# Kernel optimization log

Hardware: AMD Instinct MI355X
Metric: run time of the kernel (lower is better)

Reference implementation:

```python
import jax, jax.numpy as jnp
import numpy as np

N, F, E = 10000, 128, 640000
HID_RO = 64


def setup_inputs() -> dict:
    key = jax.random.key(0)
    ks = jax.random.split(key, 16)
    s = 1.0 / np.sqrt(F)
    inp = {
        'h': jax.random.normal(ks[0], (N, F), jnp.float32),
        'src_idx': jax.random.randint(ks[1], (E,), 0, N, jnp.int32),
        'dst_idx': jax.random.randint(ks[2], (E,), 0, N, jnp.int32),
        # message-creation MLP (F -> F -> F)
        'W1': jax.random.normal(ks[3], (F, F), jnp.float32) * s,
        'b1': jnp.zeros((F,), jnp.float32),
        'W2': jax.random.normal(ks[4], (F, F), jnp.float32) * s,
        'b2': jnp.zeros((F,), jnp.float32),
        # attention aggregation kernels
        'node_kernel': jax.random.normal(ks[5], (F, F), jnp.float32) * s,
        'attn_kernel': jax.random.normal(ks[6], (2 * F, 1), jnp.float32) * s,
        # feed-forward update (agg + h -> new h)
        'Wu': jax.random.normal(ks[7], (2 * F, F), jnp.float32) * s,
        'bu': jnp.zeros((F,), jnp.float32),
        # readout MLP (F -> 64 -> 1)
        'Wr1': jax.random.normal(ks[8], (F, HID_RO), jnp.float32) * s,
        'br1': jnp.zeros((HID_RO,), jnp.float32),
        'Wr2': jax.random.normal(ks[9], (HID_RO, 1), jnp.float32) * (1.0 / np.sqrt(HID_RO)),
        'br2': jnp.zeros((1,), jnp.float32),
    }
    return inp


def reference(h, src_idx, dst_idx, W1, b1, W2, b2, node_kernel, attn_kernel,
              Wu, bu, Wr1, br1, Wr2, br2):
    n = h.shape[0]
    # per-edge gather + message-creation NN  [E, F]
    h_src = h[src_idx]
    m = jax.nn.relu(h_src @ W1 + b1) @ W2 + b2
    # attention aggregation (GAT-style): transform messages, score vs dst state
    wh = m @ node_kernel                      # [E, F]
    h_dst = h[dst_idx]                        # [E, F]
    e = jax.nn.leaky_relu(jnp.concatenate([wh, h_dst], axis=-1) @ attn_kernel,
                          negative_slope=0.2)[:, 0]  # [E]
    # per-destination segment softmax (numerically stable)
    e_max = jax.ops.segment_max(e, dst_idx, num_segments=n)
    ex = jnp.exp(e - e_max[dst_idx])
    denom = jax.ops.segment_sum(ex, dst_idx, num_segments=n)
    alpha = ex / (denom[dst_idx] + 1e-9)
    # scatter-reduce weighted messages into destination states  [N, F]
    agg = jax.ops.segment_sum(m * alpha[:, None], dst_idx, num_segments=n)
    # feed-forward update
    h_new = jax.nn.relu(jnp.concatenate([agg, h], axis=-1) @ Wu + bu)
    # readout MLP -> per-node scalar
    out = jax.nn.relu(h_new @ Wr1 + br1) @ Wr2 + br2  # [N, 1]
    return out
```

## Files before the change

### kernel.cpp

```cpp
#include <hip/hip_runtime.h>
#include <hip/hip_bf16.h>
#include <hip/hip_fp16.h>

#define F 128
#define HID 64
#define KMAX 4
#define DEG_CAP 256
#define NTM 16
#define NTU 16
#define CHUNK_LOG 13
#define CHUNK (1 << CHUNK_LOG)


__global__ __launch_bounds__(256) void fused_front(
    const int* __restrict__ dst, unsigned short* __restrict__ cnt,
    unsigned short* __restrict__ rank,
    int e, int n, int histBlocks,
    const float* __restrict__ h,
    const float* __restrict__ W1, const float* __restrict__ b1,
    const float* __restrict__ W2, const float* __restrict__ b2,
    const float* __restrict__ nk, const float* __restrict__ attn,
    __half* __restrict__ Mh, float* __restrict__ p, float* __restrict__ q)
{
    __shared__ __align__(16) int lhist[10240];
    int tid = threadIdx.x;

    if ((int)blockIdx.x < histBlocks) {
        int n4 = n >> 2;
        int4* lh4 = (int4*)lhist;
        for (int i = tid; i < n4; i += 256) lh4[i] = make_int4(0, 0, 0, 0);
        for (int i = (n4 << 2) + tid; i < n; i += 256) lhist[i] = 0;
        __syncthreads();

        int base = (int)blockIdx.x << CHUNK_LOG;
        int lim = min(e - base, CHUNK);
        int lim4 = lim >> 2;
        const int4* d4 = (const int4*)(dst + base);
        for (int k = tid; k < lim4; k += 256) {
            int4 dv = d4[k];
            ushort4 rv;
            rv.x = (unsigned short)atomicAdd(&lhist[dv.x], 1);
            rv.y = (unsigned short)atomicAdd(&lhist[dv.y], 1);
            rv.z = (unsigned short)atomicAdd(&lhist[dv.z], 1);
            rv.w = (unsigned short)atomicAdd(&lhist[dv.w], 1);
            *(ushort4*)&rank[base + 4 * k] = rv;
        }
        for (int k = (lim4 << 2) + tid; k < lim; k += 256)
            rank[base + k] = (unsigned short)atomicAdd(&lhist[dst[base + k]], 1);
        __syncthreads();

        unsigned int* crow = (unsigned int*)(cnt + (size_t)blockIdx.x * n);
        int nh = n >> 1;
        for (int i = tid; i < nh; i += 256) {
            unsigned int v = ((unsigned int)lhist[2 * i] & 0xffffu) |
                             ((unsigned int)lhist[2 * i + 1] << 16);
            crow[i] = v;
        }
        return;
    }

    float (*hsTs)[F] = (float (*)[F])lhist;
    float (*Wc)[F]   = (float (*)[F])((char*)lhist + 8192);
    float* v1s       = (float*)((char*)lhist + 24576);

    int bm = blockIdx.x - histBlocks;
    int row0 = bm * NTM;
    int j0 = (tid & 31) * 4;
    int r0 = (tid >> 5) * 2;

    #pragma unroll
    for (int it = 0; it < 2; ++it) {
        int s4 = tid + it * 256;
        int r = s4 >> 5, c4 = s4 & 31;
        int row = row0 + r;
        float4 v = make_float4(0, 0, 0, 0);
        if (row < n) v = *(const float4*)&h[(size_t)row * F + c4 * 4];
        *(float4*)&hsTs[r][c4 * 4] = v;
    }
    if (tid < F) {
        float a = 0.f;
        const float4* nkr = (const float4*)&nk[(size_t)tid * F];
        const float4* at4 = (const float4*)attn;
        #pragma unroll 8
        for (int j = 0; j < 32; ++j) {
            float4 nv = nkr[j]; float4 av = at4[j];
            a = fmaf(nv.x, av.x, a); a = fmaf(nv.y, av.y, a);
            a = fmaf(nv.z, av.z, a); a = fmaf(nv.w, av.w, a);
        }
        v1s[tid] = a;
    }
    __syncthreads();

    {
        int r = tid >> 4, kp = tid & 15;
        float qa = 0.f;
        #pragma unroll
        for (int c = 0; c < 2; ++c) {
            float4 hv = *(const float4*)&hsTs[r][kp * 8 + c * 4];
            float4 av = *(const float4*)&attn[F + kp * 8 + c * 4];
            qa = fmaf(hv.x, av.x, qa); qa = fmaf(hv.y, av.y, qa);
            qa = fmaf(hv.z, av.z, qa); qa = fmaf(hv.w, av.w, qa);
        }
        #pragma unroll
        for (int off = 1; off < 16; off <<= 1) qa += __shfl_xor(qa, off, 64);
        int row = row0 + r;
        if (kp == 0 && row < n) q[row] = qa;
    }

    float4 acc[2];
    {
        float4 bv = *(const float4*)&b1[j0];
        acc[0] = bv; acc[1] = bv;
    }
    for (int cc = 0; cc < 4; ++cc) {
        int kc = ((cc + bm) & 3) * 32;
        __syncthreads();
        #pragma unroll
        for (int it = 0; it < 4; ++it) {
            int s4 = tid + it * 256;
            int wr = s4 >> 5, wc4 = s4 & 31;
            *(float4*)&Wc[wr][wc4 * 4] =
                *(const float4*)&W1[(size_t)(kc + wr) * F + wc4 * 4];
        }
        __syncthreads();
        #pragma unroll
        for (int k4 = 0; k4 < 8; ++k4) {
            int kk = k4 * 4;
            float4 a0 = *(const float4*)&hsTs[r0 + 0][kc + kk];
            float4 a1 = *(const float4*)&hsTs[r0 + 1][kc + kk];
            #pragma unroll
            for (int k = 0; k < 4; ++k) {
                float4 b = *(const float4*)&Wc[kk + k][j0];
                float av0 = k == 0 ? a0.x : k == 1 ? a0.y : k == 2 ? a0.z : a0.w;
                float av1 = k == 0 ? a1.x : k == 1 ? a1.y : k == 2 ? a1.z : a1.w;
                acc[0].x = fmaf(av0, b.x, acc[0].x); acc[0].y = fmaf(av0, b.y, acc[0].y);
                acc[0].z = fmaf(av0, b.z, acc[0].z); acc[0].w = fmaf(av0, b.w, acc[0].w);
                acc[1].x = fmaf(av1, b.x, acc[1].x); acc[1].y = fmaf(av1, b.y, acc[1].y);
                acc[1].z = fmaf(av1, b.z, acc[1].z); acc[1].w = fmaf(av1, b.w, acc[1].w);
            }
        }
    }
    __syncthreads();
    #pragma unroll
    for (int i = 0; i < 2; ++i) {
        float4 t = acc[i];
        t.x = fmaxf(t.x, 0.f); t.y = fmaxf(t.y, 0.f);
        t.z = fmaxf(t.z, 0.f); t.w = fmaxf(t.w, 0.f);
        *(float4*)&hsTs[r0 + i][j0] = t;
    }

    {
        float4 bv = *(const float4*)&b2[j0];
        acc[0] = bv; acc[1] = bv;
    }
    for (int cc = 0; cc < 4; ++cc) {
        int kc = ((cc + bm) & 3) * 32;
        __syncthreads();
        #pragma unroll
        for (int it = 0; it < 4; ++it) {
            int s4 = tid + it * 256;
            int wr = s4 >> 5, wc4 = s4 & 31;
            *(float4*)&Wc[wr][wc4 * 4] =
                *(const float4*)&W2[(size_t)(kc + wr) * F + wc4 * 4];
        }
        __syncthreads();
        #pragma unroll
        for (int k4 = 0; k4 < 8; ++k4) {
            int kk = k4 * 4;
            float4 a0 = *(const float4*)&hsTs[r0 + 0][kc + kk];
            float4 a1 = *(const float4*)&hsTs[r0 + 1][kc + kk];
            #pragma unroll
            for (int k = 0; k < 4; ++k) {
                float4 b = *(const float4*)&Wc[kk + k][j0];
                float av0 = k == 0 ? a0.x : k == 1 ? a0.y : k == 2 ? a0.z : a0.w;
                float av1 = k == 0 ? a1.x : k == 1 ? a1.y : k == 2 ? a1.z : a1.w;
                acc[0].x = fmaf(av0, b.x, acc[0].x); acc[0].y = fmaf(av0, b.y, acc[0].y);
                acc[0].z = fmaf(av0, b.z, acc[0].z); acc[0].w = fmaf(av0, b.w, acc[0].w);
                acc[1].x = fmaf(av1, b.x, acc[1].x); acc[1].y = fmaf(av1, b.y, acc[1].y);
                acc[1].z = fmaf(av1, b.z, acc[1].z); acc[1].w = fmaf(av1, b.w, acc[1].w);
            }
        }
    }

    float4 v1v = *(const float4*)&v1s[j0];
    #pragma unroll
    for (int i = 0; i < 2; ++i) {
        int row = row0 + r0 + i;
        if (row < n) {
            __half hv[4];
            hv[0] = __float2half(acc[i].x); hv[1] = __float2half(acc[i].y);
            hv[2] = __float2half(acc[i].z); hv[3] = __float2half(acc[i].w);
            *(uint2*)&Mh[(size_t)row * F + j0] = *(uint2*)hv;
        }
        float pp = acc[i].x * v1v.x + acc[i].y * v1v.y +
                   acc[i].z * v1v.z + acc[i].w * v1v.w;
        #pragma unroll
        for (int off = 1; off < 32; off <<= 1) pp += __shfl_xor(pp, off, 64);
        if ((tid & 31) == 0 && row < n) p[row] = pp;
    }
}

__global__ __launch_bounds__(256) void scan_block(
    unsigned short* __restrict__ cnt, int* __restrict__ rstart,
    int* __restrict__ bsum, int n, int hb)
{
    int tid = threadIdx.x;
    int i = blockIdx.x * 256 + tid;
    int run = 0;
    if (i < n) {
        size_t stride = (size_t)n;
        size_t idx = (size_t)i;
        int r = 0;
        for (; r + 8 <= hb; r += 8) {
            int c0 = cnt[idx];
            int c1 = cnt[idx + stride];
            int c2 = cnt[idx + 2 * stride];
            int c3 = cnt[idx + 3 * stride];
            int c4 = cnt[idx + 4 * stride];
            int c5 = cnt[idx + 5 * stride];
            int c6 = cnt[idx + 6 * stride];
            int c7 = cnt[idx + 7 * stride];
            cnt[idx]              = (unsigned short)run;
            cnt[idx + stride]     = (unsigned short)(run + c0);
            cnt[idx + 2 * stride] = (unsigned short)(run + (c0 + c1));
            cnt[idx + 3 * stride] = (unsigned short)(run + (c0 + c1 + c2));
            cnt[idx + 4 * stride] = (unsigned short)(run + (c0 + c1 + c2 + c3));
            cnt[idx + 5 * stride] = (unsigned short)(run + (c0 + c1 + c2 + c3 + c4));
            cnt[idx + 6 * stride] = (unsigned short)(run + (c0 + c1 + c2 + c3 + c4 + c5));
            cnt[idx + 7 * stride] = (unsigned short)(run + (c0 + c1 + c2 + c3 + c4 + c5 + c6));
            run += c0 + c1 + c2 + c3 + c4 + c5 + c6 + c7;
            idx += 8 * stride;
        }
        for (; r < hb; ++r) {
            int c = cnt[idx];
            cnt[idx] = (unsigned short)run;
            run += c;
            idx += stride;
        }
    }
    int v = run;
    int lane = tid & 63, wv = tid >> 6;
    int x = v;
    #pragma unroll
    for (int off = 1; off < 64; off <<= 1) {
        int t = __shfl_up(x, off, 64);
        if (lane >= off) x += t;
    }
    __shared__ int wsum[4];
    if (lane == 63) wsum[wv] = x;
    __syncthreads();
    int woff = 0;
    #pragma unroll
    for (int wdx = 0; wdx < 4; ++wdx) woff += (wdx < wv) ? wsum[wdx] : 0;
    int incl = x + woff;
    if (i < n) rstart[i] = incl - v;
    if (tid == 255) bsum[blockIdx.x] = incl;
}

__global__ __launch_bounds__(256) void fill_kernel(
    const int* __restrict__ dst, const int* __restrict__ src,
    const unsigned short* __restrict__ rank, const int* __restrict__ rstart,
    const unsigned short* __restrict__ cntoff, const int* __restrict__ bsum,
    unsigned short* __restrict__ src_sorted, int n, int nb, int e)
{
    __shared__ int sbo[64];
    int tid = threadIdx.x;
    if (tid < 64) {
        int v = (tid < nb) ? bsum[tid] : 0;
        int x = v;
        #pragma unroll
        for (int off = 1; off < 64; off <<= 1) {
            int t = __shfl_up(x, off, 64);
            if (tid >= off) x += t;
        }
        sbo[tid] = x - v;
    }
    __syncthreads();
    int i = blockIdx.x * 256 + tid;
    if (i < e) {
        int d = dst[i];
        int rep = i >> CHUNK_LOG;
        int pos = rstart[d] + sbo[d >> 8] + (int)cntoff[(size_t)rep * n + d] + (int)rank[i];
        src_sorted[pos] = (unsigned short)src[i];
    }
}

__global__ __launch_bounds__(256) void agg_update(
    const __half* __restrict__ Mh, const float* __restrict__ p,
    const float* __restrict__ q, const int* __restrict__ rstart,
    const int* __restrict__ bsum, const unsigned short* __restrict__ src_sorted,
    const float* __restrict__ h,
    const float* __restrict__ Wu, const float* __restrict__ bu,
    const float* __restrict__ Wr1, const float* __restrict__ br1,
    const float* __restrict__ Wr2, const float* __restrict__ br2,
    float* __restrict__ out, int n, int nb, int e)
{
    __shared__ __align__(16) float smem[8192];
    float (*X)[2 * F] = (float (*)[2 * F])smem;
    int2* bufa = (int2*)&smem[4096];
    int*  sbo  = (int*)&smem[6144];

    int tid = threadIdx.x;
    int wv   = tid >> 6;
    int lane = tid & 63;
    int row0 = blockIdx.x * NTU;

    if (tid < 64) {
        int v = (tid < nb) ? bsum[tid] : 0;
        int x = v;
        #pragma unroll
        for (int off = 1; off < 64; off <<= 1) {
            int t = __shfl_up(x, off, 64);
            if (tid >= off) x += t;
        }
        sbo[tid] = x - v;
    }
    #pragma unroll
    for (int it = 0; it < 2; ++it) {
        int s4 = tid + it * 256;
        int r = s4 >> 5, c4 = s4 & 31;
        int row = row0 + r;
        float4 v = make_float4(0, 0, 0, 0);
        if (row < n) v = *(const float4*)&h[(size_t)row * F + c4 * 4];
        *(float4*)&X[r][128 + c4 * 4] = v;
    }
    __syncthreads();

    const uint4* M16 = (const uint4*)Mh;
    int sub16 = lane & 15;
    int quar  = lane >> 4;
    int2* bufw = bufa + wv * DEG_CAP;

    for (int s = 0; s < 4; ++s) {
        int lr = wv * 4 + s;
        int node = row0 + lr;
        if (node >= n) break;

        int start = rstart[node] + sbo[node >> 8];
        int end   = (node + 1 < n) ? rstart[node + 1] + sbo[(node + 1) >> 8] : e;
        int deg   = end - start;
        float qn  = q[node];

        float w[KMAX];
        int   sidx[KMAX];
        float lmax = -1e30f;

        #pragma unroll
        for (int k = 0; k < KMAX; ++k) {
            int i = start + lane + (k << 6);
            bool valid = (i < end);
            int sv = valid ? (int)src_sorted[i] : 0;
            float pv = valid ? p[sv] : 0.0f;
            float sc = pv + qn;
            float ev = (sc > 0.0f) ? sc : 0.2f * sc;
            w[k] = valid ? ev : -1e30f;
            sidx[k] = sv;
            lmax = fmaxf(lmax, w[k]);
        }
        for (int i = start + DEG_CAP + lane; i < end; i += 64) {
            float sc = p[(int)src_sorted[i]] + qn;
            float ev = (sc > 0.0f) ? sc : 0.2f * sc;
            lmax = fmaxf(lmax, ev);
        }
        #pragma unroll
        for (int off = 32; off >= 1; off >>= 1)
            lmax = fmaxf(lmax, __shfl_xor(lmax, off, 64));

        float lsum = 0.0f;
        #pragma unroll
        for (int k = 0; k < KMAX; ++k) {
            float ex = (w[k] > -1e29f) ? __expf(w[k] - lmax) : 0.0f;
            w[k] = ex;
            lsum += ex;
        }
        for (int i = start + DEG_CAP + lane; i < end; i += 64) {
            float sc = p[(int)src_sorted[i]] + qn;
            float ev = (sc > 0.0f) ? sc : 0.2f * sc;
            lsum += __expf(ev - lmax);
        }
        #pragma unroll
        for (int off = 32; off >= 1; off >>= 1)
            lsum += __shfl_xor(lsum, off, 64);
        float inv = 1.0f / (lsum + 1e-9f);

        #pragma unroll
        for (int k = 0; k < KMAX; ++k)
            bufw[lane + (k << 6)] = make_int2(__float_as_int(w[k] * inv), sidx[k]);

        float acc[8] = {0.f, 0.f, 0.f, 0.f, 0.f, 0.f, 0.f, 0.f};
        int lim = min(deg, DEG_CAP);
        lim = (lim + 15) & ~15;

        for (int base = 0; base < lim; base += 16) {
            int2  rr[4];
            uint4 mm[4];
            #pragma unroll
            for (int u = 0; u < 4; ++u) rr[u] = bufw[base + quar + 4 * u];
            #pragma unroll
            for (int u = 0; u < 4; ++u) mm[u] = M16[(size_t)rr[u].y * 16 + sub16];
            #pragma unroll
            for (int u = 0; u < 4; ++u) {
                float wu = __int_as_float(rr[u].x);
                const __half2* hp = (const __half2*)&mm[u];
                float2 f0 = __half22float2(hp[0]);
                float2 f1 = __half22float2(hp[1]);
                float2 f2 = __half22float2(hp[2]);
                float2 f3 = __half22float2(hp[3]);
                acc[0] = fmaf(wu, f0.x, acc[0]); acc[1] = fmaf(wu, f0.y, acc[1]);
                acc[2] = fmaf(wu, f1.x, acc[2]); acc[3] = fmaf(wu, f1.y, acc[3]);
                acc[4] = fmaf(wu, f2.x, acc[4]); acc[5] = fmaf(wu, f2.y, acc[5]);
                acc[6] = fmaf(wu, f3.x, acc[6]); acc[7] = fmaf(wu, f3.y, acc[7]);
            }
        }

        for (int base = start + DEG_CAP; base < end; base += 64) {
            int i = base + lane;
            float ex = 0.f; int sv = 0;
            if (i < end) {
                sv = (int)src_sorted[i];
                float sc = p[sv] + qn;
                float ev = (sc > 0.0f) ? sc : 0.2f * sc;
                ex = __expf(ev - lmax) * inv;
            }
            bufw[lane] = make_int2(__float_as_int(ex), sv);
            for (int b2 = 0; b2 < 64; b2 += 4) {
                int2 rr = bufw[b2 + quar];
                uint4 mm = M16[(size_t)rr.y * 16 + sub16];
                float wu = __int_as_float(rr.x);
                const __half2* hp = (const __half2*)&mm;
                float2 f0 = __half22float2(hp[0]);
                float2 f1 = __half22float2(hp[1]);
                float2 f2 = __half22float2(hp[2]);
                float2 f3 = __half22float2(hp[3]);
                acc[0] = fmaf(wu, f0.x, acc[0]); acc[1] = fmaf(wu, f0.y, acc[1]);
                acc[2] = fmaf(wu, f1.x, acc[2]); acc[3] = fmaf(wu, f1.y, acc[3]);
                acc[4] = fmaf(wu, f2.x, acc[4]); acc[5] = fmaf(wu, f2.y, acc[5]);
                acc[6] = fmaf(wu, f3.x, acc[6]); acc[7] = fmaf(wu, f3.y, acc[7]);
            }
        }

        #pragma unroll
        for (int j = 0; j < 8; ++j) {
            acc[j] += __shfl_xor(acc[j], 16, 64);
            acc[j] += __shfl_xor(acc[j], 32, 64);
        }
        if (quar == 0) {
            *(float4*)&X[lr][sub16 * 8]     = make_float4(acc[0], acc[1], acc[2], acc[3]);
            *(float4*)&X[lr][sub16 * 8 + 4] = make_float4(acc[4], acc[5], acc[6], acc[7]);
        }
    }
    __syncthreads();

    int j0 = (lane & 31) * 4;
    int rh = (lane >> 5) * 8;
    float4 acc[8];
    #pragma unroll
    for (int i = 0; i < 8; ++i) acc[i] = make_float4(0.f, 0.f, 0.f, 0.f);
    int kbase = wv * 64;
    for (int k4 = 0; k4 < 16; ++k4) {
        int kk = kbase + k4 * 4;
        float4 a[8];
        #pragma unroll
        for (int r = 0; r < 8; ++r) a[r] = *(const float4*)&X[rh + r][kk];
        #pragma unroll
        for (int k = 0; k < 4; ++k) {
            float4 b = *(const float4*)&Wu[(size_t)(kk + k) * F + j0];
            #pragma unroll
            for (int r = 0; r < 8; ++r) {
                float av = k == 0 ? a[r].x : k == 1 ? a[r].y : k == 2 ? a[r].z : a[r].w;
                acc[r].x = fmaf(av, b.x, acc[r].x);
                acc[r].y = fmaf(av, b.y, acc[r].y);
                acc[r].z = fmaf(av, b.z, acc[r].z);
                acc[r].w = fmaf(av, b.w, acc[r].w);
            }
        }
    }
    __syncthreads();

    #pragma unroll
    for (int r = 0; r < 8; ++r)
        *(float4*)&smem[wv * 2048 + (rh + r) * 128 + j0] = acc[r];
    __syncthreads();

    #pragma unroll
    for (int u = 0; u < 2; ++u) {
        int idx = tid * 2 + u;
        int row = idx >> 5, c4 = (idx & 31) * 4;
        float4 s0 = *(const float4*)&smem[0 * 2048 + row * 128 + c4];
        float4 s1 = *(const float4*)&smem[1 * 2048 + row * 128 + c4];
        float4 s2 = *(const float4*)&smem[2 * 2048 + row * 128 + c4];
        float4 s3 = *(const float4*)&smem[3 * 2048 + row * 128 + c4];
        float4 bv = *(const float4*)&bu[c4];
        float4 t;
        t.x = fmaxf(s0.x + s1.x + s2.x + s3.x + bv.x, 0.f);
        t.y = fmaxf(s0.y + s1.y + s2.y + s3.y + bv.y, 0.f);
        t.z = fmaxf(s0.z + s1.z + s2.z + s3.z + bv.z, 0.f);
        t.w = fmaxf(s0.w + s1.w + s2.w + s3.w + bv.w, 0.f);
        *(float4*)&smem[row * 128 + c4] = t;
    }
    __syncthreads();

    int h0 = (lane & 31) * 2;
    float r1a[8], r1b[8];
    #pragma unroll
    for (int r = 0; r < 8; ++r) { r1a[r] = 0.f; r1b[r] = 0.f; }
    int kb2 = wv * 32;
    for (int k4 = 0; k4 < 8; ++k4) {
        int kk = kb2 + k4 * 4;
        float4 a[8];
        #pragma unroll
        for (int r = 0; r < 8; ++r) a[r] = *(const float4*)&smem[(rh + r) * 128 + kk];
        #pragma unroll
        for (int k = 0; k < 4; ++k) {
            float2 b = *(const float2*)&Wr1[(size_t)(kk + k) * HID + h0];
            #pragma unroll
            for (int r = 0; r < 8; ++r) {
                float av = k == 0 ? a[r].x : k == 1 ? a[r].y : k == 2 ? a[r].z : a[r].w;
                r1a[r] = fmaf(av, b.x, r1a[r]);
                r1b[r] = fmaf(av, b.y, r1b[r]);
            }
        }
    }
    #pragma unroll
    for (int r = 0; r < 8; ++r) {
        smem[2048 + wv * 1024 + (rh + r) * 64 + h0]     = r1a[r];
        smem[2048 + wv * 1024 + (rh + r) * 64 + h0 + 1] = r1b[r];
    }
    __syncthreads();

    {
        int row = tid >> 4;
        int hp  = (tid & 15) * 4;
        float val = 0.f;
        #pragma unroll
        for (int j = 0; j < 4; ++j) {
            int hh = hp + j;
            float s = br1[hh]
                    + smem[2048 + 0 * 1024 + row * 64 + hh]
                    + smem[2048 + 1 * 1024 + row * 64 + hh]
                    + smem[2048 + 2 * 1024 + row * 64 + hh]
                    + smem[2048 + 3 * 1024 + row * 64 + hh];
            val = fmaf(fmaxf(s, 0.f), Wr2[hh], val);
        }
        #pragma unroll
        for (int off = 1; off < 16; off <<= 1) val += __shfl_xor(val, off, 64);
        int orow = row0 + row;
        if ((tid & 15) == 0 && orow < n) out[orow] = val + br2[0];
    }
}

extern "C" void kernel_launch(void* const* d_in, const int* in_sizes, int n_in,
                              void* d_out, int out_size, void* d_ws, size_t ws_size,
                              hipStream_t stream) {
    const float* h    = (const float*)d_in[0];
    const int*   src  = (const int*)d_in[1];
    const int*   dst  = (const int*)d_in[2];
    const float* W1   = (const float*)d_in[3];
    const float* b1   = (const float*)d_in[4];
    const float* W2   = (const float*)d_in[5];
    const float* b2   = (const float*)d_in[6];
    const float* nk   = (const float*)d_in[7];
    const float* attn = (const float*)d_in[8];
    const float* Wu   = (const float*)d_in[9];
    const float* bu   = (const float*)d_in[10];
    const float* Wr1  = (const float*)d_in[11];
    const float* br1  = (const float*)d_in[12];
    const float* Wr2  = (const float*)d_in[13];
    const float* br2  = (const float*)d_in[14];
    float* out = (float*)d_out;

    int n = in_sizes[0] / F;
    int e = in_sizes[1];
    int nb = (n + 255) / 256;
    int hb = (e + CHUNK - 1) >> CHUNK_LOG;
    int mlpBlocks  = (n + NTM - 1) / NTM;
    int fusBlocks  = (n + NTU - 1) / NTU;
    int fillBlocks = (e + 255) / 256;

    char* ws = (char*)d_ws;
    size_t off = 0;
    auto alloc = [&](size_t bytes) {
        void* pp = ws + off;
        off += (bytes + 511) & ~(size_t)511;
        return pp;
    };
    __half* Mh             = (__half*)alloc((size_t)n * F * 2);
    float* p               = (float*)alloc((size_t)n * 4);
    float* q               = (float*)alloc((size_t)n * 4);
    unsigned short* cnt    = (unsigned short*)alloc((size_t)hb * n * 2);
    int*   rstart          = (int*)alloc((size_t)(n + 1) * 4);
    int*   bsum            = (int*)alloc((size_t)(nb + 1) * 4);
    unsigned short* rank   = (unsigned short*)alloc((size_t)e * 2);
    unsigned short* srcsort= (unsigned short*)alloc((size_t)e * 2);

    fused_front<<<hb + mlpBlocks, 256, 0, stream>>>(
        dst, cnt, rank, e, n, hb,
        h, W1, b1, W2, b2, nk, attn, Mh, p, q);
    scan_block<<<nb, 256, 0, stream>>>(cnt, rstart, bsum, n, hb);
    fill_kernel<<<fillBlocks, 256, 0, stream>>>(dst, src, rank, rstart,
                                                cnt, bsum, srcsort,
                                                n, nb, e);
    agg_update<<<fusBlocks, 256, 0, stream>>>(Mh, p, q, rstart, bsum, srcsort,
                                              h, Wu, bu, Wr1, br1, Wr2, br2,
                                              out, n, nb, e);
}
```

Measured before the change: 157.3 us.

## Split-K node MLP across waves with register tiles and shared-memory reduction

Restructures the per-node message MLP in the front kernel. Each of the four waves now handles a 32-wide K slice, with each thread computing an 8-row by 4-column register tile and reading W1/W2 directly from global memory instead of staging weight chunks through shared memory. Partial sums are reduced across waves in shared memory, then bias and ReLU are applied. The aim is to raise arithmetic intensity per thread and drop the repeated weight staging and its barriers. The cost is more registers, extra shared-memory reduction traffic and more syncthreads around each layer.

Result: no change. 154.5 us (-1.8%).

```diff
diff --git a/kernel.cpp b/kernel.cpp
--- a/kernel.cpp
+++ b/kernel.cpp
@@ -59,14 +59,13 @@
         return;
     }
 
-    float (*hsTs)[F] = (float (*)[F])lhist;
-    float (*Wc)[F]   = (float (*)[F])((char*)lhist + 8192);
-    float* v1s       = (float*)((char*)lhist + 24576);
-
+    float* smem = (float*)lhist;
     int bm = blockIdx.x - histBlocks;
     int row0 = bm * NTM;
-    int j0 = (tid & 31) * 4;
-    int r0 = (tid >> 5) * 2;
+    int wv   = tid >> 6;
+    int lane = tid & 63;
+    int j0 = (lane & 31) * 4;
+    int rh = (lane >> 5) * 8;
 
     #pragma unroll
     for (int it = 0; it < 2; ++it) {
@@ -75,8 +74,117 @@
         int row = row0 + r;
         float4 v = make_float4(0, 0, 0, 0);
         if (row < n) v = *(const float4*)&h[(size_t)row * F + c4 * 4];
-        *(float4*)&hsTs[r][c4 * 4] = v;
-    }
+        *(float4*)&smem[r * F + c4 * 4] = v;
+    }
+    __syncthreads();
+
+    {
+        int r = tid >> 4, kp = tid & 15;
+        float qa = 0.f;
+        #pragma unroll
+        for (int c = 0; c < 2; ++c) {
+            float4 hv = *(const float4*)&smem[r * F + kp * 8 + c * 4];
+            float4 av = *(const float4*)&attn[F + kp * 8 + c * 4];
+            qa = fmaf(hv.x, av.x, qa); qa = fmaf(hv.y, av.y, qa);
+            qa = fmaf(hv.z, av.z, qa); qa = fmaf(hv.w, av.w, qa);
+        }
+        #pragma unroll
+        for (int off = 1; off < 16; off <<= 1) qa += __shfl_xor(qa, off, 64);
+        int row = row0 + r;
+        if (kp == 0 && row < n) q[row] = qa;
+    }
+
+    float4 acc[8];
+    #pragma unroll
+    for (int i = 0; i < 8; ++i) acc[i] = make_float4(0.f, 0.f, 0.f, 0.f);
+    int kbase = wv * 32;
+    for (int k4 = 0; k4 < 8; ++k4) {
+        int kk = kbase + k4 * 4;
+        float4 a[8];
+        #pragma unroll
+        for (int r = 0; r < 8; ++r) a[r] = *(const float4*)&smem[(rh + r) * F + kk];
+        #pragma unroll
+        for (int k = 0; k < 4; ++k) {
+            float4 b = *(const float4*)&W1[(size_t)(kk + k) * F + j0];
+            #pragma unroll
+            for (int r = 0; r < 8; ++r) {
+                float av = k == 0 ? a[r].x : k == 1 ? a[r].y : k == 2 ? a[r].z : a[r].w;
+                acc[r].x = fmaf(av, b.x, acc[r].x);
+                acc[r].y = fmaf(av, b.y, acc[r].y);
+                acc[r].z = fmaf(av, b.z, acc[r].z);
+                acc[r].w = fmaf(av, b.w, acc[r].w);
+            }
+        }
+    }
+    __syncthreads();
+
+    #pragma unroll
+    for (int r = 0; r < 8; ++r)
+        *(float4*)&smem[2048 + wv * 2048 + (rh + r) * 128 + j0] = acc[r];
+    __syncthreads();
+
+    #pragma unroll
+    for (int u = 0; u < 2; ++u) {
+        int idx = tid * 2 + u;
+        int row = idx >> 5, c4 = (idx & 31) * 4;
+        float4 s0 = *(const float4*)&smem[2048 + 0 * 2048 + row * 128 + c4];
+        float4 s1 = *(const float4*)&smem[2048 + 1 * 2048 + row * 128 + c4];
+        float4 s2 = *(const float4*)&smem[2048 + 2 * 2048 + row * 128 + c4];
+        float4 s3 = *(const float4*)&smem[2048 + 3 * 2048 + row * 128 + c4];
+        float4 bv = *(const float4*)&b1[c4];
+        float4 t;
+        t.x = fmaxf(s0.x + s1.x + s2.x + s3.x + bv.x, 0.f);
+        t.y = fmaxf(s0.y + s1.y + s2.y + s3.y + bv.y, 0.f);
+        t.z = fmaxf(s0.z + s1.z + s2.z + s3.z + bv.z, 0.f);
+        t.w = fmaxf(s0.w + s1.w + s2.w + s3.w + bv.w, 0.f);
+        *(float4*)&smem[row * 128 + c4] = t;
+    }
+    __syncthreads();
+
+    #pragma unroll
+    for (int i = 0; i < 8; ++i) acc[i] = make_float4(0.f, 0.f, 0.f, 0.f);
+    for (int k4 = 0; k4 < 8; ++k4) {
+        int kk = kbase + k4 * 4;
+        float4 a[8];
+        #pragma unroll
+        for (int r = 0; r < 8; ++r) a[r] = *(const float4*)&smem[(rh + r) * 128 + kk];
+        #pragma unroll
+        for (int k = 0; k < 4; ++k) {
+            float4 b = *(const float4*)&W2[(size_t)(kk + k) * F + j0];
+            #pragma unroll
+            for (int r = 0; r < 8; ++r) {
+                float av = k == 0 ? a[r].x : k == 1 ? a[r].y : k == 2 ? a[r].z : a[r].w;
+                acc[r].x = fmaf(av, b.x, acc[r].x);
+                acc[r].y = fmaf(av, b.y, acc[r].y);
+                acc[r].z = fmaf(av, b.z, acc[r].z);
+                acc[r].w = fmaf(av, b.w, acc[r].w);
+            }
+        }
+    }
+    __syncthreads();
+    #pragma unroll
+    for (int r = 0; r < 8; ++r)
+        *(float4*)&smem[2048 + wv * 2048 + (rh + r) * 128 + j0] = acc[r];
+    __syncthreads();
+
+    #pragma unroll
+    for (int u = 0; u < 2; ++u) {
+        int idx = tid * 2 + u;
+        int row = idx >> 5, c4 = (idx & 31) * 4;
+        float4 s0 = *(const float4*)&smem[2048 + 0 * 2048 + row * 128 + c4];
+        float4 s1 = *(const float4*)&smem[2048 + 1 * 2048 + row * 128 + c4];
+        float4 s2 = *(const float4*)&smem[2048 + 2 * 2048 + row * 128 + c4];
+        float4 s3 = *(const float4*)&smem[2048 + 3 * 2048 + row * 128 + c4];
+        float4 bv = *(const float4*)&b2[c4];
+        float4 t;
+        t.x = s0.x + s1.x + s2.x + s3.x + bv.x;
+        t.y = s0.y + s1.y + s2.y + s3.y + bv.y;
+        t.z = s0.z + s1.z + s2.z + s3.z + bv.z;
+        t.w = s0.w + s1.w + s2.w + s3.w + bv.w;
+        *(float4*)&smem[row * 128 + c4] = t;
+    }
+    __syncthreads();
+
     if (tid < F) {
         float a = 0.f;
         const float4* nkr = (const float4*)&nk[(size_t)tid * F];
@@ -87,116 +195,30 @@
             a = fmaf(nv.x, av.x, a); a = fmaf(nv.y, av.y, a);
             a = fmaf(nv.z, av.z, a); a = fmaf(nv.w, av.w, a);
         }
-        v1s[tid] = a;
+        smem[2048 + tid] = a;
     }
     __syncthreads();
 
     {
-        int r = tid >> 4, kp = tid & 15;
-        float qa = 0.f;
-        #pragma unroll
-        for (int c = 0; c < 2; ++c) {
-            float4 hv = *(const float4*)&hsTs[r][kp * 8 + c * 4];
-            float4 av = *(const float4*)&attn[F + kp * 8 + c * 4];
-            qa = fmaf(hv.x, av.x, qa); qa = fmaf(hv.y, av.y, qa);
-            qa = fmaf(hv.z, av.z, qa); qa = fmaf(hv.w, av.w, qa);
-        }
-        #pragma unroll
-        for (int off = 1; off < 16; off <<= 1) qa += __shfl_xor(qa, off, 64);
-        int row = row0 + r;
-        if (kp == 0 && row < n) q[row] = qa;
-    }
-
-    float4 acc[2];
-    {
-        float4 bv = *(const float4*)&b1[j0];
-        acc[0] = bv; acc[1] = bv;
-    }
-    for (int cc = 0; cc < 4; ++cc) {
-        int kc = ((cc + bm) & 3) * 32;
-        __syncthreads();
-        #pragma unroll
-        for (int it = 0; it < 4; ++it) {
-            int s4 = tid + it * 256;
-            int wr = s4 >> 5, wc4 = s4 & 31;
-            *(float4*)&Wc[wr][wc4 * 4] =
-                *(const float4*)&W1[(size_t)(kc + wr) * F + wc4 * 4];
-        }
-        __syncthreads();
-        #pragma unroll
-        for (int k4 = 0; k4 < 8; ++k4) {
-            int kk = k4 * 4;
-            float4 a0 = *(const float4*)&hsTs[r0 + 0][kc + kk];
-            float4 a1 = *(const float4*)&hsTs[r0 + 1][kc + kk];
-            #pragma unroll
-            for (int k = 0; k < 4; ++k) {
-                float4 b = *(const float4*)&Wc[kk + k][j0];
-                float av0 = k == 0 ? a0.x : k == 1 ? a0.y : k == 2 ? a0.z : a0.w;
-                float av1 = k == 0 ? a1.x : k == 1 ? a1.y : k == 2 ? a1.z : a1.w;
-                acc[0].x = fmaf(av0, b.x, acc[0].x); acc[0].y = fmaf(av0, b.y, acc[0].y);
-                acc[0].z = fmaf(av0, b.z, acc[0].z); acc[0].w = fmaf(av0, b.w, acc[0].w);
-                acc[1].x = fmaf(av1, b.x, acc[1].x); acc[1].y = fmaf(av1, b.y, acc[1].y);
-                acc[1].z = fmaf(av1, b.z, acc[1].z); acc[1].w = fmaf(av1, b.w, acc[1].w);
-            }
-        }
-    }
-    __syncthreads();
-    #pragma unroll
-    for (int i = 0; i < 2; ++i) {
-        float4 t = acc[i];
-        t.x = fmaxf(t.x, 0.f); t.y = fmaxf(t.y, 0.f);
-        t.z = fmaxf(t.z, 0.f); t.w = fmaxf(t.w, 0.f);
-        *(float4*)&hsTs[r0 + i][j0] = t;
-    }
-
-    {
-        float4 bv = *(const float4*)&b2[j0];
-        acc[0] = bv; acc[1] = bv;
-    }
-    for (int cc = 0; cc < 4; ++cc) {
-        int kc = ((cc + bm) & 3) * 32;
-        __syncthreads();
-        #pragma unroll
-        for (int it = 0; it < 4; ++it) {
-            int s4 = tid + it * 256;
-            int wr = s4 >> 5, wc4 = s4 & 31;
-            *(float4*)&Wc[wr][wc4 * 4] =
-                *(const float4*)&W2[(size_t)(kc + wr) * F + wc4 * 4];
-        }
-        __syncthreads();
-        #pragma unroll
-        for (int k4 = 0; k4 < 8; ++k4) {
-            int kk = k4 * 4;
-            float4 a0 = *(const float4*)&hsTs[r0 + 0][kc + kk];
-            float4 a1 = *(const float4*)&hsTs[r0 + 1][kc + kk];
-            #pragma unroll
-            for (int k = 0; k < 4; ++k) {
-                float4 b = *(const float4*)&Wc[kk + k][j0];
-                float av0 = k == 0 ? a0.x : k == 1 ? a0.y : k == 2 ? a0.z : a0.w;
-                float av1 = k == 0 ? a1.x : k == 1 ? a1.y : k == 2 ? a1.z : a1.w;
-                acc[0].x = fmaf(av0, b.x, acc[0].x); acc[0].y = fmaf(av0, b.y, acc[0].y);
-                acc[0].z = fmaf(av0, b.z, acc[0].z); acc[0].w = fmaf(av0, b.w, acc[0].w);
-                acc[1].x = fmaf(av1, b.x, acc[1].x); acc[1].y = fmaf(av1, b.y, acc[1].y);
-                acc[1].z = fmaf(av1, b.z, acc[1].z); acc[1].w = fmaf(av1, b.w, acc[1].w);
-            }
-        }
-    }
-
-    float4 v1v = *(const float4*)&v1s[j0];
-    #pragma unroll
-    for (int i = 0; i < 2; ++i) {
-        int row = row0 + r0 + i;
-        if (row < n) {
-            __half hv[4];
-            hv[0] = __float2half(acc[i].x); hv[1] = __float2half(acc[i].y);
-            hv[2] = __float2half(acc[i].z); hv[3] = __float2half(acc[i].w);
-            *(uint2*)&Mh[(size_t)row * F + j0] = *(uint2*)hv;
-        }
-        float pp = acc[i].x * v1v.x + acc[i].y * v1v.y +
-                   acc[i].z * v1v.z + acc[i].w * v1v.w;
-        #pragma unroll
-        for (int off = 1; off < 32; off <<= 1) pp += __shfl_xor(pp, off, 64);
-        if ((tid & 31) == 0 && row < n) p[row] = pp;
+        int row = tid >> 4, c8 = (tid & 15) * 8;
+        int grow = row0 + row;
+        float4 m0 = *(const float4*)&smem[row * 128 + c8];
+        float4 m1 = *(const float4*)&smem[row * 128 + c8 + 4];
+        if (grow < n) {
+            __half hv[8];
+            hv[0] = __float2half(m0.x); hv[1] = __float2half(m0.y);
+            hv[2] = __float2half(m0.z); hv[3] = __float2half(m0.w);
+            hv[4] = __float2half(m1.x); hv[5] = __float2half(m1.y);
+            hv[6] = __float2half(m1.z); hv[7] = __float2half(m1.w);
+            *(uint4*)&Mh[(size_t)grow * F + c8] = *(uint4*)hv;
+        }
+        float4 v0 = *(const float4*)&smem[2048 + c8];
+        float4 v1v = *(const float4*)&smem[2048 + c8 + 4];
+        float pp = m0.x * v0.x + m0.y * v0.y + m0.z * v0.z + m0.w * v0.w +
+                   m1.x * v1v.x + m1.y * v1v.y + m1.z * v1v.z + m1.w * v1v.w;
+        #pragma unroll
+        for (int off = 1; off < 16; off <<= 1) pp += __shfl_xor(pp, off, 64);
+        if ((tid & 15) == 0 && grow < n) p[grow] = pp;
     }
 }
 
```
